# Performance work log

Measured on AMD Instinct MI355X. Metric: run time of the kernel, lower is better.

The kernel has to match this reference:

```python
import jax, jax.numpy as jnp
import numpy as np
from jax import lax

MAX_BOXES = 1000
IOU_THRESHOLD = 0.5
SCORE_THRESHOLD = 0.3
N_BOXES = 300000
N_FEAT = 85  # 4 box + 1 conf + 80 classes


def setup_inputs() -> dict:
    key = jax.random.key(0)
    inputs = jax.random.uniform(key, (N_BOXES, N_FEAT), dtype=jnp.float32)
    return {"inputs": inputs}


def _nms_indices(boxes, scores, max_boxes, iou_thr):
    """Fixed-size greedy NMS (tf.image.non_max_suppression semantics).
    Returns (idxs[max_boxes] int32, valid[max_boxes] bool). Padded slots invalid.
    Indices are non-differentiable, matching TF."""
    boxes = lax.stop_gradient(boxes)
    scores = lax.stop_gradient(scores)
    y1, x1, y2, x2 = boxes[:, 0], boxes[:, 1], boxes[:, 2], boxes[:, 3]
    areas = (y2 - y1) * (x2 - x1)

    def step(cur_scores, _):
        idx = jnp.argmax(cur_scores)
        valid = jnp.isfinite(cur_scores[idx])
        b = boxes[idx]
        iy1 = jnp.maximum(b[0], y1)
        ix1 = jnp.maximum(b[1], x1)
        iy2 = jnp.minimum(b[2], y2)
        ix2 = jnp.minimum(b[3], x2)
        inter = jnp.maximum(iy2 - iy1, 0.0) * jnp.maximum(ix2 - ix1, 0.0)
        union = areas[idx] + areas - inter
        iou = jnp.where(union > 0, inter / union, 0.0)
        suppress = (iou > iou_thr) & valid
        new_scores = jnp.where(suppress, -jnp.inf, cur_scores)
        new_scores = new_scores.at[idx].set(-jnp.inf)
        return new_scores, (idx.astype(jnp.int32), valid)

    _, (idxs, valids) = lax.scan(step, scores, None, length=max_boxes)
    return idxs, valids


def reference(inputs):
    boxes = inputs[..., 0:4]                      # [N,4]
    box_confidence = inputs[..., 4:5]             # [N,1]
    box_class_probs = inputs[..., 5:]             # [N,C]
    box_scores = box_confidence * box_class_probs # [N,C]
    box_classes = jnp.argmax(box_scores, axis=-1)        # [N]
    box_class_scores = jnp.max(box_scores, axis=-1)      # [N]
    # boolean_mask emulated by sending failing scores to -inf (fixed shape)
    keep = box_class_scores >= SCORE_THRESHOLD
    masked_scores = jnp.where(keep, box_class_scores, -jnp.inf)

    idxs, valids = _nms_indices(boxes, masked_scores, MAX_BOXES, IOU_THRESHOLD)

    out_boxes = boxes[idxs]                                  # [max_boxes,4]
    out_scores = box_class_scores[idxs][:, None]             # [max_boxes,1]
    out_classes = box_classes[idxs].astype(jnp.float32)[:, None]
    out = jnp.concatenate([out_boxes, out_classes, out_scores], axis=-1)  # [max_boxes,6]
    # zero padded (invalid) rows; original returned variable-length [k,6]
    return jnp.where(valids[:, None], out, 0.0)
```

## Files before the change

kernel.cpp:

```cpp
#include <hip/hip_runtime.h>

#define NBOX 300000
#define NFEAT 85
#define NCLS 80
#define NBUCK 4096
#define HSPLIT 16
#define CMAX 8192
#define W64 (CMAX / 64)
#define MAXKEEP 1000
#define SC_ROWS 64

typedef unsigned long long u64;
typedef float f4a __attribute__((ext_vector_type(4), aligned(16)));

__device__ __forceinline__ int bucket_of(float s) {
    int b = (int)((s - 0.3f) * (4096.0f / 0.7f));
    if (b < 0) b = 0;
    if (b > NBUCK - 1) b = NBUCK - 1;
    return b;
}

__device__ __forceinline__ bool sup_iou(float by1, float bx1, float by2, float bx2, float ba,
                                        float y1, float x1, float y2, float x2, float area) {
    float iy1 = fmaxf(by1, y1), ix1 = fmaxf(bx1, x1);
    float iy2 = fminf(by2, y2), ix2 = fminf(bx2, x2);
    float inter = fmaxf(iy2 - iy1, 0.0f) * fmaxf(ix2 - ix1, 0.0f);
    float uni = ba + area - inter;
    float iou = (uni > 0.0f) ? inter / uni : 0.0f;
    return iou > 0.5f;
}

__global__ void k_init(unsigned* __restrict__ hist16, unsigned* __restrict__ cnt,
                       int* __restrict__ meta) {
    int i = blockIdx.x * blockDim.x + threadIdx.x;
    if (i < HSPLIT * NBUCK) hist16[i] = 0u;
    if (i < NBUCK) cnt[i] = 0u;
    if (i < 16) meta[i] = 0;
}

__global__ void __launch_bounds__(256) k_scores(const float* __restrict__ in,
        float* __restrict__ scores, unsigned* __restrict__ hist16) {
    __shared__ float lds[SC_ROWS * NFEAT];
    int t = threadIdx.x;
    long long rbase = (long long)blockIdx.x * SC_ROWS;
    int rows = (NBOX - rbase < SC_ROWS) ? (int)(NBOX - rbase) : SC_ROWS;
    int nfl = rows * NFEAT;
    int nf4 = nfl >> 2;
    const f4a* src = (const f4a*)(in + rbase * NFEAT);
    f4a* dst = (f4a*)lds;
    for (int k = t; k < nf4; k += 256) dst[k] = src[k];
    for (int k = (nf4 << 2) + t; k < nfl; k += 256) lds[k] = in[rbase * NFEAT + k];
    __syncthreads();
    unsigned* myhist = hist16 + (size_t)(blockIdx.x & (HSPLIT - 1)) * NBUCK;
    int row = t >> 2, part = t & 3;
    if (row < rows) {
        const float* r = lds + row * NFEAT;
        const float* p = r + 5 + 20 * part;
        float mx = p[0];
        #pragma unroll
        for (int j = 1; j < 20; ++j) mx = fmaxf(mx, p[j]);
        mx = fmaxf(mx, __shfl_xor(mx, 1));
        mx = fmaxf(mx, __shfl_xor(mx, 2));
        if (part == 0) {
            float best = r[4] * mx;
            scores[rbase + row] = best;
            if (best >= 0.3f) atomicAdd(&myhist[bucket_of(best)], 1u);
        }
    }
}

__global__ void __launch_bounds__(1024) k_thresh(const unsigned* __restrict__ hist16,
        unsigned* __restrict__ histsum, unsigned* __restrict__ off, int* __restrict__ meta) {
    __shared__ unsigned chunk[1024];
    int t = threadIdx.x;
    unsigned h[4];
    unsigned s = 0;
    #pragma unroll
    for (int j = 0; j < 4; ++j) {
        unsigned v = 0;
        for (int g = 0; g < HSPLIT; ++g) v += hist16[g * NBUCK + t * 4 + j];
        h[j] = v; histsum[t * 4 + j] = v; s += v;
    }
    chunk[t] = s;
    __syncthreads();
    for (int o = 1; o < 1024; o <<= 1) {
        unsigned add = (t + o < 1024) ? chunk[t + o] : 0u;
        __syncthreads();
        chunk[t] += add;
        __syncthreads();
    }
    unsigned after = (t + 1 < 1024) ? chunk[t + 1] : 0u;
    unsigned suf[5];
    suf[4] = after;
    #pragma unroll
    for (int j = 3; j >= 0; --j) suf[j] = suf[j + 1] + h[j];
    #pragma unroll
    for (int j = 0; j < 4; ++j) {
        int b = t * 4 + j;
        off[b] = suf[j] - h[j];
        unsigned sufb = suf[j], sufprev;
        if (b == 0) sufprev = 0xFFFFFFFFu;
        else if (j > 0) sufprev = suf[j - 1];
        else {
            unsigned hprev = 0;
            for (int g = 0; g < HSPLIT; ++g) hprev += hist16[g * NBUCK + b - 1];
            sufprev = sufb + hprev;
        }
        if (sufb <= (unsigned)CMAX && sufprev > (unsigned)CMAX) {
            meta[1] = b;
            meta[0] = (int)sufb;
        }
    }
}

__global__ void k_scatter(const float* __restrict__ scores, const int* __restrict__ meta,
                          const unsigned* __restrict__ off, unsigned* __restrict__ cnt,
                          u64* __restrict__ unsorted) {
    int i = blockIdx.x * blockDim.x + threadIdx.x;
    if (i >= NBOX) return;
    float s = scores[i];
    if (s < 0.3f) return;
    int b = bucket_of(s);
    if (b < meta[1]) return;
    unsigned slot = off[b] + atomicAdd(&cnt[b], 1u);
    if (slot < CMAX)
        unsorted[slot] = ((u64)__float_as_uint(s) << 32) |
                         (u64)(0xFFFFFFFFu - (unsigned)i);
}

__global__ void k_rank(const float* __restrict__ in, const u64* __restrict__ unsorted,
                       const unsigned* __restrict__ off, const unsigned* __restrict__ histsum,
                       const int* __restrict__ meta, u64* __restrict__ sorted,
                       float4* __restrict__ boxes4, unsigned* __restrict__ vflag) {
    int i = blockIdx.x * blockDim.x + threadIdx.x;
    int total = meta[0];
    if (i >= total) return;
    u64 k = unsorted[i];
    float s = __uint_as_float((unsigned)(k >> 32));
    int b = bucket_of(s);
    unsigned base = off[b];
    unsigned n = histsum[b];
    unsigned r = 0;
    for (unsigned u = 0; u < n; ++u) r += (unsorted[base + u] > k) ? 1u : 0u;
    int bi = (int)(0xFFFFFFFFu - (unsigned)(k & 0xFFFFFFFFull));
    const float* p = in + (size_t)bi * NFEAT;
    float4 bx = make_float4(p[0], p[1], p[2], p[3]);
    sorted[base + r] = k;
    boxes4[base + r] = bx;
    vflag[base + r] = (bx.z > bx.x && bx.w > bx.y) ? 1u : 0u;
}

__global__ void __launch_bounds__(1024) k_nms(const float4* __restrict__ boxes4,
        const unsigned* __restrict__ vflag, int* __restrict__ meta,
        unsigned* __restrict__ vincl, unsigned* __restrict__ cmap,
        float4* __restrict__ cboxes, int* __restrict__ kfinal) {
    __shared__ float4 klist[MAXKEEP + 64];
    __shared__ u64 colmask[64];
    __shared__ u64 pf[16];
    __shared__ u64 vkeptw[W64];
    __shared__ unsigned wsum[16];
    __shared__ int sh_nkept, sh_wlim, sh_stop;
    int t = threadIdx.x;
    int lane = t & 63, wv = t >> 6;
    int total = meta[0];

    if (t < W64) vkeptw[t] = 0ull;
    if (t == 0) { sh_nkept = 0; sh_wlim = 0; sh_stop = 0; }

    unsigned f[8];
    {
        unsigned run = 0;
        #pragma unroll
        for (int e = 0; e < 8; ++e) {
            int s = t * 8 + e;
            unsigned v = (s < total) ? vflag[s] : 0u;
            run += v;
            f[e] = run;
        }
        unsigned wx = run;
        #pragma unroll
        for (int o = 1; o < 64; o <<= 1) {
            unsigned u = __shfl_up(wx, o);
            if (lane >= o) wx += u;
        }
        if (lane == 63) wsum[wv] = wx;
        __syncthreads();
        if (t < 16) {
            unsigned v = wsum[t];
            #pragma unroll
            for (int o = 1; o < 16; o <<= 1) {
                unsigned u = __shfl_up(v, o);
                if (t >= o) v += u;
            }
            wsum[t] = v;
        }
        __syncthreads();
        unsigned base = ((wv > 0) ? wsum[wv - 1] : 0u) + (wx - run);
        #pragma unroll
        for (int e = 0; e < 8; ++e) {
            int s = t * 8 + e;
            unsigned incl = base + f[e];
            vincl[s] = incl;
            if (s < total && vflag[s]) {
                cmap[incl - 1] = (unsigned)s;
                cboxes[incl - 1] = boxes4[s];
            }
        }
    }
    int nv = (int)wsum[15];
    if (t == 0) meta[3] = nv;
    int nblkv = (nv + 63) >> 6;
    __syncthreads();

    for (int w = 0; w < nblkv; ++w) {
        int base = w << 6;
        int c = base + lane;
        float4 mb = (c < nv) ? cboxes[c] : make_float4(0.f, 0.f, 0.f, 0.f);
        float marea = (mb.z - mb.x) * (mb.w - mb.y);
        int cend = (base + 63 < nv - 1) ? (base + 63) : (nv - 1);
        unsigned cm = 0;
        if (wv == 0) cm = cmap[cend];
        int nk = sh_nkept;
        bool ok = true;
        for (int k = wv; k < nk; k += 16) {
            float4 b = klist[k];
            float ba = (b.z - b.x) * (b.w - b.y);
            if (sup_iou(b.x, b.y, b.z, b.w, ba, mb.x, mb.y, mb.z, mb.w, marea))
                ok = false;
        }
        u64 pv = __ballot(ok ? 1 : 0);
        if (lane == 0) pf[wv] = pv;
        #pragma unroll
        for (int r = 0; r < 4; ++r) {
            int i = wv * 4 + r;
            int ii = (base + i < nv) ? (base + i) : 0;
            float4 bi = cboxes[ii];
            float ba = (bi.z - bi.x) * (bi.w - bi.y);
            bool s = (lane > i) &&
                     sup_iou(bi.x, bi.y, bi.z, bi.w, ba, mb.x, mb.y, mb.z, mb.w, marea);
            u64 bm = __ballot(s ? 1 : 0);
            if (lane == 0) colmask[i] = bm;
        }
        __syncthreads();
        if (wv == 0) {
            int rc = nv - base;
            u64 vm = (rc >= 64) ? ~0ull : ((1ull << rc) - 1ull);
            u64 aliveM = vm;
            #pragma unroll
            for (int q = 0; q < 16; ++q) aliveM &= pf[q];
            u64 col = colmask[lane];
            u64 nzc = __ballot(col != 0ull);
            u64 remaining = aliveM, keptM = 0ull;
            while (remaining) {
                u64 hard = remaining & nzc;
                if (!hard) { keptM |= remaining; break; }
                int ih = __ffsll(hard) - 1;
                u64 below = remaining & ((1ull << ih) - 1ull);
                keptM |= below | (1ull << ih);
                remaining &= ~(below | (1ull << ih));
                u64 ci = __shfl(col, ih);
                remaining &= ~ci;
            }
            int nk0 = sh_nkept;
            if ((keptM >> lane) & 1ull) {
                int rank = __popcll(keptM & ((1ull << lane) - 1ull));
                klist[nk0 + rank] = mb;
            }
            if (lane == 0) {
                int kp = __popcll(keptM);
                vkeptw[w] = keptM;
                sh_nkept = nk0 + kp;
                sh_wlim = w + 1;
                if ((int)cm - cend + nk0 + kp >= MAXKEEP) sh_stop = 1;
            }
        }
        __syncthreads();
        if (sh_stop) break;
    }
    int wlim = sh_wlim;

    {
        unsigned run = 0;
        #pragma unroll
        for (int e = 0; e < 8; ++e) {
            int s = t * 8 + e;
            unsigned kept = 0u;
            if (s < total) {
                if (!vflag[s]) kept = 1u;
                else {
                    unsigned cc = vincl[s] - 1u;
                    int w = (int)(cc >> 6);
                    if (w < wlim && ((vkeptw[w] >> (cc & 63u)) & 1ull)) kept = 1u;
                }
            }
            run += kept;
            f[e] = run;
        }
        unsigned wx = run;
        #pragma unroll
        for (int o = 1; o < 64; o <<= 1) {
            unsigned u = __shfl_up(wx, o);
            if (lane >= o) wx += u;
        }
        __syncthreads();
        if (lane == 63) wsum[wv] = wx;
        __syncthreads();
        if (t < 16) {
            unsigned v = wsum[t];
            #pragma unroll
            for (int o = 1; o < 16; o <<= 1) {
                unsigned u = __shfl_up(v, o);
                if (t >= o) v += u;
            }
            wsum[t] = v;
        }
        __syncthreads();
        unsigned base = ((wv > 0) ? wsum[wv - 1] : 0u) + (wx - run);
        #pragma unroll
        for (int e = 0; e < 8; ++e) {
            int s = t * 8 + e;
            unsigned kept = 0u;
            if (s < total) {
                if (!vflag[s]) kept = 1u;
                else {
                    unsigned cc = vincl[s] - 1u;
                    int w = (int)(cc >> 6);
                    if (w < wlim && ((vkeptw[w] >> (cc & 63u)) & 1ull)) kept = 1u;
                }
            }
            unsigned incl = base + f[e];
            if (kept && incl <= (unsigned)MAXKEEP) kfinal[incl - 1] = s;
        }
        if (t == 0) {
            unsigned tot = wsum[15];
            meta[2] = (int)(tot < (unsigned)MAXKEEP ? tot : (unsigned)MAXKEEP);
        }
    }
}

__global__ void __launch_bounds__(256) k_output(const float* __restrict__ in,
        const u64* __restrict__ gkeys, const int* __restrict__ meta,
        const int* __restrict__ kfinal, float* __restrict__ out) {
    int gw = (blockIdx.x * blockDim.x + threadIdx.x) >> 6;
    int lane = threadIdx.x & 63;
    if (gw >= MAXKEEP) return;
    int kc = meta[2];
    if (gw < kc) {
        int pos = kfinal[gw];
        u64 key = gkeys[pos];
        int bi = (int)(0xFFFFFFFFu - (unsigned)(key & 0xFFFFFFFFull));
        const float* row = in + (size_t)bi * NFEAT;
        float conf = row[4];
        float v0 = (lane < NCLS) ? conf * row[5 + lane] : -1.0f;
        float v1 = (lane < NCLS - 64) ? conf * row[5 + 64 + lane] : -1.0f;
        float bv = (v1 > v0) ? v1 : v0;
        int bix = (v1 > v0) ? (64 + lane) : lane;
        #pragma unroll
        for (int o = 1; o < 64; o <<= 1) {
            float ov = __shfl_xor(bv, o);
            int oi = __shfl_xor(bix, o);
            if (ov > bv || (ov == bv && oi < bix)) { bv = ov; bix = oi; }
        }
        float wv = 0.f;
        if (lane < 4) wv = row[lane];
        else if (lane == 4) wv = (float)bix;
        else wv = bv;
        if (lane < 6) out[gw * 6 + lane] = wv;
    } else {
        if (lane < 6) out[gw * 6 + lane] = 0.f;
    }
}

extern "C" void kernel_launch(void* const* d_in, const int* in_sizes, int n_in,
                              void* d_out, int out_size, void* d_ws, size_t ws_size,
                              hipStream_t stream) {
    const float* in = (const float*)d_in[0];
    float* out = (float*)d_out;
    char* ws = (char*)d_ws;
    u64* sorted = (u64*)(ws);
    int* meta = (int*)(ws + 65536);
    int* kfinal = (int*)(ws + 65600);
    unsigned* vflag = (unsigned*)(ws + 69696);
    unsigned* vincl = (unsigned*)(ws + 102464);
    unsigned* cmap = (unsigned*)(ws + 135232);
    float4* cboxes = (float4*)(ws + 168000);
    float4* boxes4 = (float4*)(ws + 300096);
    float* scores = (float*)(ws + 431168);
    unsigned* hist16 = (unsigned*)(ws + 1631168);
    unsigned* histsum = (unsigned*)(ws + 1893312);
    unsigned* cnt = (unsigned*)(ws + 1909696);
    unsigned* off = (unsigned*)(ws + 1926080);
    u64* unsorted = (u64*)(ws + 1942464);

    k_init<<<dim3(256), dim3(256), 0, stream>>>(hist16, cnt, meta);
    k_scores<<<dim3((NBOX + SC_ROWS - 1) / SC_ROWS), dim3(256), 0, stream>>>(in, scores, hist16);
    k_thresh<<<dim3(1), dim3(1024), 0, stream>>>(hist16, histsum, off, meta);
    k_scatter<<<dim3((NBOX + 255) / 256), dim3(256), 0, stream>>>(scores, meta, off, cnt, unsorted);
    k_rank<<<dim3(CMAX / 256), dim3(256), 0, stream>>>(in, unsorted, off, histsum, meta, sorted, boxes4, vflag);
    k_nms<<<dim3(1), dim3(1024), 0, stream>>>(boxes4, vflag, meta, vincl, cmap, cboxes, kfinal);
    k_output<<<dim3((MAXKEEP * 64 + 255) / 256), dim3(256), 0, stream>>>(in, sorted, meta, kfinal, out);
}
```

Baseline: 109.4 us.

## Fuse threshold, rank and output stages into neighbouring kernels to cut launches

The histogram threshold/prefix step moves into the last block of k_scores, chosen with an atomic ticket counter, so its separate single-block launch disappears. The bucket rank-sort moves into the start of the single-block NMS kernel, and the final output gather moves onto its tail. This cuts the launch count from seven to four to remove launch gaps, but the rank and output work now run on one 1024-thread block instead of many blocks. The ticket counter in meta[8] depends on k_init zeroing it each call.

```diff
diff --git a/kernel.cpp b/kernel.cpp
--- a/kernel.cpp
+++ b/kernel.cpp
@@ -9,6 +9,7 @@
 #define W64 (CMAX / 64)
 #define MAXKEEP 1000
 #define SC_ROWS 64
+#define NBLKS ((NBOX + SC_ROWS - 1) / SC_ROWS)
 
 typedef unsigned long long u64;
 typedef float f4a __attribute__((ext_vector_type(4), aligned(16)));
@@ -30,6 +31,10 @@
     return iou > 0.5f;
 }
 
+__device__ __forceinline__ unsigned cload(const unsigned* p) {
+    return __hip_atomic_load(p, __ATOMIC_RELAXED, __HIP_MEMORY_SCOPE_AGENT);
+}
+
 __global__ void k_init(unsigned* __restrict__ hist16, unsigned* __restrict__ cnt,
                        int* __restrict__ meta) {
     int i = blockIdx.x * blockDim.x + threadIdx.x;
@@ -39,8 +44,12 @@
 }
 
 __global__ void __launch_bounds__(256) k_scores(const float* __restrict__ in,
-        float* __restrict__ scores, unsigned* __restrict__ hist16) {
+        float* __restrict__ scores, unsigned* __restrict__ hist16,
+        unsigned* __restrict__ histsum, unsigned* __restrict__ off,
+        int* __restrict__ meta) {
     __shared__ float lds[SC_ROWS * NFEAT];
+    __shared__ unsigned chunk[256];
+    __shared__ int sh_last;
     int t = threadIdx.x;
     long long rbase = (long long)blockIdx.x * SC_ROWS;
     int rows = (NBOX - rbase < SC_ROWS) ? (int)(NBOX - rbase) : SC_ROWS;
@@ -67,43 +76,46 @@
             if (best >= 0.3f) atomicAdd(&myhist[bucket_of(best)], 1u);
         }
     }
-}
-
-__global__ void __launch_bounds__(1024) k_thresh(const unsigned* __restrict__ hist16,
-        unsigned* __restrict__ histsum, unsigned* __restrict__ off, int* __restrict__ meta) {
-    __shared__ unsigned chunk[1024];
-    int t = threadIdx.x;
-    unsigned h[4];
+    __syncthreads();
+    if (t == 0) {
+        __threadfence();
+        unsigned tk = atomicAdd((unsigned*)&meta[8], 1u);
+        sh_last = (tk == (unsigned)(NBLKS - 1)) ? 1 : 0;
+    }
+    __syncthreads();
+    if (!sh_last) return;
+    unsigned h[16];
     unsigned s = 0;
     #pragma unroll
-    for (int j = 0; j < 4; ++j) {
+    for (int j = 0; j < 16; ++j) {
+        int b = t * 16 + j;
         unsigned v = 0;
-        for (int g = 0; g < HSPLIT; ++g) v += hist16[g * NBUCK + t * 4 + j];
-        h[j] = v; histsum[t * 4 + j] = v; s += v;
+        for (int g = 0; g < HSPLIT; ++g) v += cload(&hist16[g * NBUCK + b]);
+        h[j] = v; histsum[b] = v; s += v;
     }
     chunk[t] = s;
     __syncthreads();
-    for (int o = 1; o < 1024; o <<= 1) {
-        unsigned add = (t + o < 1024) ? chunk[t + o] : 0u;
+    for (int o = 1; o < 256; o <<= 1) {
+        unsigned add = (t + o < 256) ? chunk[t + o] : 0u;
         __syncthreads();
         chunk[t] += add;
         __syncthreads();
     }
-    unsigned after = (t + 1 < 1024) ? chunk[t + 1] : 0u;
-    unsigned suf[5];
-    suf[4] = after;
+    unsigned after = (t + 1 < 256) ? chunk[t + 1] : 0u;
+    unsigned suf[17];
+    suf[16] = after;
     #pragma unroll
-    for (int j = 3; j >= 0; --j) suf[j] = suf[j + 1] + h[j];
+    for (int j = 15; j >= 0; --j) suf[j] = suf[j + 1] + h[j];
     #pragma unroll
-    for (int j = 0; j < 4; ++j) {
-        int b = t * 4 + j;
-        off[b] = suf[j] - h[j];
+    for (int j = 0; j < 16; ++j) {
+        int b = t * 16 + j;
+        off[b] = suf[j + 1];
         unsigned sufb = suf[j], sufprev;
         if (b == 0) sufprev = 0xFFFFFFFFu;
         else if (j > 0) sufprev = suf[j - 1];
         else {
             unsigned hprev = 0;
-            for (int g = 0; g < HSPLIT; ++g) hprev += hist16[g * NBUCK + b - 1];
+            for (int g = 0; g < HSPLIT; ++g) hprev += cload(&hist16[g * NBUCK + b - 1]);
             sufprev = sufb + hprev;
         }
         if (sufb <= (unsigned)CMAX && sufprev > (unsigned)CMAX) {
@@ -128,32 +140,13 @@
                          (u64)(0xFFFFFFFFu - (unsigned)i);
 }
 
-__global__ void k_rank(const float* __restrict__ in, const u64* __restrict__ unsorted,
-                       const unsigned* __restrict__ off, const unsigned* __restrict__ histsum,
-                       const int* __restrict__ meta, u64* __restrict__ sorted,
-                       float4* __restrict__ boxes4, unsigned* __restrict__ vflag) {
-    int i = blockIdx.x * blockDim.x + threadIdx.x;
-    int total = meta[0];
-    if (i >= total) return;
-    u64 k = unsorted[i];
-    float s = __uint_as_float((unsigned)(k >> 32));
-    int b = bucket_of(s);
-    unsigned base = off[b];
-    unsigned n = histsum[b];
-    unsigned r = 0;
-    for (unsigned u = 0; u < n; ++u) r += (unsorted[base + u] > k) ? 1u : 0u;
-    int bi = (int)(0xFFFFFFFFu - (unsigned)(k & 0xFFFFFFFFull));
-    const float* p = in + (size_t)bi * NFEAT;
-    float4 bx = make_float4(p[0], p[1], p[2], p[3]);
-    sorted[base + r] = k;
-    boxes4[base + r] = bx;
-    vflag[base + r] = (bx.z > bx.x && bx.w > bx.y) ? 1u : 0u;
-}
-
-__global__ void __launch_bounds__(1024) k_nms(const float4* __restrict__ boxes4,
-        const unsigned* __restrict__ vflag, int* __restrict__ meta,
-        unsigned* __restrict__ vincl, unsigned* __restrict__ cmap,
-        float4* __restrict__ cboxes, int* __restrict__ kfinal) {
+__global__ void __launch_bounds__(1024) k_nms(const float* __restrict__ in,
+        const u64* __restrict__ unsorted, const unsigned* __restrict__ off,
+        const unsigned* __restrict__ histsum, int* __restrict__ meta,
+        u64* __restrict__ sorted, float4* __restrict__ boxes4,
+        unsigned* __restrict__ vflag, unsigned* __restrict__ vincl,
+        unsigned* __restrict__ cmap, float4* __restrict__ cboxes,
+        int* __restrict__ kfinal, float* __restrict__ out) {
     __shared__ float4 klist[MAXKEEP + 64];
     __shared__ u64 colmask[64];
     __shared__ u64 pf[16];
@@ -166,6 +159,23 @@
 
     if (t < W64) vkeptw[t] = 0ull;
     if (t == 0) { sh_nkept = 0; sh_wlim = 0; sh_stop = 0; }
+
+    for (int i = t; i < total; i += 1024) {
+        u64 k = unsorted[i];
+        float s = __uint_as_float((unsigned)(k >> 32));
+        int b = bucket_of(s);
+        unsigned base = off[b];
+        unsigned n = histsum[b];
+        unsigned r = 0;
+        for (unsigned u = 0; u < n; ++u) r += (unsorted[base + u] > k) ? 1u : 0u;
+        int bi = (int)(0xFFFFFFFFu - (unsigned)(k & 0xFFFFFFFFull));
+        const float* p = in + (size_t)bi * NFEAT;
+        float4 bx = make_float4(p[0], p[1], p[2], p[3]);
+        sorted[base + r] = k;
+        boxes4[base + r] = bx;
+        vflag[base + r] = (bx.z > bx.x && bx.w > bx.y) ? 1u : 0u;
+    }
+    __syncthreads();
 
     unsigned f[8];
     {
@@ -331,43 +341,37 @@
             unsigned incl = base + f[e];
             if (kept && incl <= (unsigned)MAXKEEP) kfinal[incl - 1] = s;
         }
-        if (t == 0) {
-            unsigned tot = wsum[15];
-            meta[2] = (int)(tot < (unsigned)MAXKEEP ? tot : (unsigned)MAXKEEP);
-        }
-    }
-}
-
-__global__ void __launch_bounds__(256) k_output(const float* __restrict__ in,
-        const u64* __restrict__ gkeys, const int* __restrict__ meta,
-        const int* __restrict__ kfinal, float* __restrict__ out) {
-    int gw = (blockIdx.x * blockDim.x + threadIdx.x) >> 6;
-    int lane = threadIdx.x & 63;
-    if (gw >= MAXKEEP) return;
-    int kc = meta[2];
-    if (gw < kc) {
-        int pos = kfinal[gw];
-        u64 key = gkeys[pos];
-        int bi = (int)(0xFFFFFFFFu - (unsigned)(key & 0xFFFFFFFFull));
-        const float* row = in + (size_t)bi * NFEAT;
-        float conf = row[4];
-        float v0 = (lane < NCLS) ? conf * row[5 + lane] : -1.0f;
-        float v1 = (lane < NCLS - 64) ? conf * row[5 + 64 + lane] : -1.0f;
-        float bv = (v1 > v0) ? v1 : v0;
-        int bix = (v1 > v0) ? (64 + lane) : lane;
-        #pragma unroll
-        for (int o = 1; o < 64; o <<= 1) {
-            float ov = __shfl_xor(bv, o);
-            int oi = __shfl_xor(bix, o);
-            if (ov > bv || (ov == bv && oi < bix)) { bv = ov; bix = oi; }
-        }
-        float wv = 0.f;
-        if (lane < 4) wv = row[lane];
-        else if (lane == 4) wv = (float)bix;
-        else wv = bv;
-        if (lane < 6) out[gw * 6 + lane] = wv;
-    } else {
-        if (lane < 6) out[gw * 6 + lane] = 0.f;
+    }
+    __syncthreads();
+    int kc = (int)wsum[15];
+    if (kc > MAXKEEP) kc = MAXKEEP;
+    if (t == 0) meta[2] = kc;
+
+    for (int gw = wv; gw < MAXKEEP; gw += 16) {
+        if (gw < kc) {
+            int pos = kfinal[gw];
+            u64 key = sorted[pos];
+            int bi = (int)(0xFFFFFFFFu - (unsigned)(key & 0xFFFFFFFFull));
+            const float* row = in + (size_t)bi * NFEAT;
+            float conf = row[4];
+            float v0 = (lane < NCLS) ? conf * row[5 + lane] : -1.0f;
+            float v1 = (lane < NCLS - 64) ? conf * row[5 + 64 + lane] : -1.0f;
+            float bv = (v1 > v0) ? v1 : v0;
+            int bix = (v1 > v0) ? (64 + lane) : lane;
+            #pragma unroll
+            for (int o = 1; o < 64; o <<= 1) {
+                float ov = __shfl_xor(bv, o);
+                int oi = __shfl_xor(bix, o);
+                if (ov > bv || (ov == bv && oi < bix)) { bv = ov; bix = oi; }
+            }
+            float wvv = 0.f;
+            if (lane < 4) wvv = row[lane];
+            else if (lane == 4) wvv = (float)bix;
+            else wvv = bv;
+            if (lane < 6) out[gw * 6 + lane] = wvv;
+        } else {
+            if (lane < 6) out[gw * 6 + lane] = 0.f;
+        }
     }
 }
 
@@ -393,10 +397,9 @@
     u64* unsorted = (u64*)(ws + 1942464);
 
     k_init<<<dim3(256), dim3(256), 0, stream>>>(hist16, cnt, meta);
-    k_scores<<<dim3((NBOX + SC_ROWS - 1) / SC_ROWS), dim3(256), 0, stream>>>(in, scores, hist16);
-    k_thresh<<<dim3(1), dim3(1024), 0, stream>>>(hist16, histsum, off, meta);
+    k_scores<<<dim3(NBLKS), dim3(256), 0, stream>>>(in, scores, hist16, histsum, off, meta);
     k_scatter<<<dim3((NBOX + 255) / 256), dim3(256), 0, stream>>>(scores, meta, off, cnt, unsorted);
-    k_rank<<<dim3(CMAX / 256), dim3(256), 0, stream>>>(in, unsorted, off, histsum, meta, sorted, boxes4, vflag);
-    k_nms<<<dim3(1), dim3(1024), 0, stream>>>(boxes4, vflag, meta, vincl, cmap, cboxes, kfinal);
-    k_output<<<dim3((MAXKEEP * 64 + 255) / 256), dim3(256), 0, stream>>>(in, sorted, meta, kfinal, out);
-}
+    k_nms<<<dim3(1), dim3(1024), 0, stream>>>(in, unsorted, off, histsum, meta,
+                                              sorted, boxes4, vflag, vincl, cmap,
+                                              cboxes, kfinal, out);
+}
```

Result: slower. 399.3 us (+265.1%).
